# Kernel tuning notes

Measured on AMD Instinct MI355X. Metric: run time of the kernel, lower is better.

The kernel has to match this reference:

```python
import jax, jax.numpy as jnp
import numpy as np

N_NODES = 100000
N_EDGES = 1600000
IN_C, HID_C, OUT_C = 64, 64, 32


def setup_inputs() -> dict:
    key = jax.random.key(0)
    ks = jax.random.split(key, 10)
    return {
        "x": jax.random.normal(ks[0], (N_NODES, IN_C), dtype=jnp.float32),
        "edge_index": jax.random.randint(ks[1], (2, N_EDGES), 0, N_NODES, dtype=jnp.int32),
        "W_l": jax.random.normal(ks[2], (IN_C, HID_C), dtype=jnp.float32) * 0.1,
        "W_r": jax.random.normal(ks[3], (IN_C, HID_C), dtype=jnp.float32) * 0.1,
        "b1": jax.random.normal(ks[4], (HID_C,), dtype=jnp.float32) * 0.1,
        "W_g": jax.random.normal(ks[5], (HID_C, OUT_C), dtype=jnp.float32) * 0.1,
        "att_src": jax.random.normal(ks[6], (OUT_C,), dtype=jnp.float32) * 0.1,
        "att_dst": jax.random.normal(ks[7], (OUT_C,), dtype=jnp.float32) * 0.1,
        "b2": jax.random.normal(ks[8], (OUT_C,), dtype=jnp.float32) * 0.1,
    }


def _gnn(x, edge_index, W_l, W_r, b1, W_g, att_src, att_dst, b2):
    n = x.shape[0]
    src, dst = edge_index[0], edge_index[1]

    # --- SAGEConv: mean neighbor aggregation + root transform ---
    deg = jax.ops.segment_sum(jnp.ones_like(src, dtype=x.dtype), dst, num_segments=n)
    agg = jax.ops.segment_sum(x[src], dst, num_segments=n)  # [N, IN_C]
    agg = agg / jnp.maximum(deg, 1.0)[:, None]
    h = agg @ W_l + b1 + x @ W_r
    h = jax.nn.relu(h)
    # dropout(p=0.5) is identity in eval mode

    # --- GATConv (heads=1), with self-loops (PyG default) ---
    loop = jnp.arange(n, dtype=src.dtype)
    s = jnp.concatenate([src, loop])
    d = jnp.concatenate([dst, loop])
    z = h @ W_g                      # [N, OUT_C]
    a_s = z @ att_src                # [N] per-node source score
    a_d = z @ att_dst                # [N] per-node dest score
    e = jax.nn.leaky_relu(a_s[s] + a_d[d], negative_slope=0.2)  # [E+N]
    # segment softmax over edges grouped by destination node
    m = jax.ops.segment_max(e, d, num_segments=n)
    ex = jnp.exp(e - m[d])
    denom = jax.ops.segment_sum(ex, d, num_segments=n)
    alpha = ex / denom[d]
    out = jax.ops.segment_sum(alpha[:, None] * z[s], d, num_segments=n) + b2

    return jax.nn.log_softmax(out, axis=1)


def reference(x, edge_index, W_l, W_r, b1, W_g, att_src, att_dst, b2):
    return _gnn(x, edge_index, W_l, W_r, b1, W_g, att_src, att_dst, b2)
```

## Files before the change

kernel.cpp:

```cpp
#include <hip/hip_runtime.h>
#include <cstdint>
#include <cstddef>


typedef unsigned short ushort_t;
typedef unsigned int uint_t;
typedef __attribute__((ext_vector_type(8))) short short8;
typedef __attribute__((ext_vector_type(4))) float f32x4;
typedef __attribute__((ext_vector_type(2))) float f32x2;

__device__ inline ushort_t f2bf(float f) {
    uint_t u = __float_as_uint(f);
    uint_t r = (u + 0x7fffu + ((u >> 16) & 1u)) >> 16;
    return (ushort_t)r;
}
__device__ inline float bf_lo(uint_t u) { return __uint_as_float(u << 16); }
__device__ inline float bf_hi(uint_t u) { return __uint_as_float(u & 0xffff0000u); }

#define PART_CHUNK 8192


__global__ __launch_bounds__(256) void k_cnt(const int* __restrict__ ei, int* __restrict__ tot, int E, int NB) {
    __shared__ int h[512];
    int tid = threadIdx.x;
    for (int b = tid; b < NB; b += 256) h[b] = 0;
    __syncthreads();
    int b0 = blockIdx.x * PART_CHUNK;
    int b1 = min(b0 + PART_CHUNK, E);
    for (int j = b0 + tid; j < b1; j += 256) atomicAdd(&h[ei[E + j] >> 8], 1);
    __syncthreads();
    for (int b = tid; b < NB; b += 256) if (h[b]) atomicAdd(&tot[b], h[b]);
}

__global__ __launch_bounds__(256) void k_scan(const int* __restrict__ tot, int* __restrict__ base,
                                              int* __restrict__ gofs, int* __restrict__ rowptr,
                                              int NB, int E, int N) {
    __shared__ int t[256];
    int tid = threadIdx.x;
    int v0 = (2 * tid < NB) ? tot[2 * tid] : 0;
    int v1 = (2 * tid + 1 < NB) ? tot[2 * tid + 1] : 0;
    t[tid] = v0 + v1;
    __syncthreads();
    for (int off = 1; off < 256; off <<= 1) {
        int u = (tid >= off) ? t[tid - off] : 0;
        __syncthreads();
        t[tid] += u;
        __syncthreads();
    }
    int pairExcl = (tid > 0) ? t[tid - 1] : 0;
    if (2 * tid < NB)     { base[2 * tid] = pairExcl;          gofs[2 * tid] = pairExcl; }
    if (2 * tid + 1 < NB) { base[2 * tid + 1] = pairExcl + v0; gofs[2 * tid + 1] = pairExcl + v0; }
    if (tid == 0) { rowptr[N] = E; base[NB] = E; }
}

__global__ __launch_bounds__(256) void k_part(const int* __restrict__ ei, int* __restrict__ gofs,
                                              uint_t* __restrict__ pairs, int E, int NB) {
    __shared__ int h[512];
    __shared__ int ofs[512];
    int tid = threadIdx.x;
    for (int b = tid; b < NB; b += 256) h[b] = 0;
    __syncthreads();
    int b0 = blockIdx.x * PART_CHUNK;
    int b1 = min(b0 + PART_CHUNK, E);
    for (int j = b0 + tid; j < b1; j += 256) atomicAdd(&h[ei[E + j] >> 8], 1);
    __syncthreads();
    for (int b = tid; b < NB; b += 256) ofs[b] = h[b] ? atomicAdd(&gofs[b], h[b]) : 0;
    __syncthreads();
    for (int j = b0 + tid; j < b1; j += 256) {
        int d = ei[E + j], s = ei[j];
        int p = atomicAdd(&ofs[d >> 8], 1);
        pairs[p] = (uint_t)s | ((uint_t)(d & 255) << 24);
    }
}

__global__ __launch_bounds__(256) void k_csr(const uint_t* __restrict__ pairs, const int* __restrict__ base,
                                             int* __restrict__ rowptr, int* __restrict__ csr, int N) {
    __shared__ int h[256];
    __shared__ int s[256];
    int b = blockIdx.x;
    int d0 = b << 8;
    int e0 = base[b], e1 = base[b + 1];
    int tid = threadIdx.x;
    h[tid] = 0;
    __syncthreads();
    for (int j = e0 + tid; j < e1; j += 256) atomicAdd(&h[pairs[j] >> 24], 1);
    __syncthreads();
    int v = h[tid];
    s[tid] = v;
    __syncthreads();
    for (int off = 1; off < 256; off <<= 1) {
        int u = (tid >= off) ? s[tid - off] : 0;
        __syncthreads();
        s[tid] += u;
        __syncthreads();
    }
    int excl = s[tid] - v;
    int d = d0 + tid;
    if (d < N) rowptr[d] = e0 + excl;
    __syncthreads();
    h[tid] = e0 + excl;
    __syncthreads();
    for (int j = e0 + tid; j < e1; j += 256) {
        uint_t p = pairs[j];
        int pos = atomicAdd(&h[p >> 24], 1);
        csr[pos] = (int)(p & 0xffffffu);
    }
}


__global__ __launch_bounds__(256) void k_cvt(const float* __restrict__ x, ushort_t* __restrict__ xh,
                                             unsigned char* __restrict__ xq, int n4) {
    int idx = blockIdx.x * 256 + threadIdx.x;
    if (idx < n4) {
        float4 v = ((const float4*)x)[idx];
        ushort4 o = { f2bf(v.x), f2bf(v.y), f2bf(v.z), f2bf(v.w) };
        ((ushort4*)xh)[idx] = o;
        int r = 0;
        r = __builtin_amdgcn_cvt_pk_fp8_f32(v.x, v.y, r, false);
        r = __builtin_amdgcn_cvt_pk_fp8_f32(v.z, v.w, r, true);
        ((uint_t*)xq)[idx] = (uint_t)r;
    }
}

__global__ __launch_bounds__(256) void k_wcvt(const float* __restrict__ Wl, const float* __restrict__ Wr,
                                              const float* __restrict__ Wg,
                                              ushort_t* __restrict__ Wlrt, ushort_t* __restrict__ Wgt) {
    int t = blockIdx.x * 256 + threadIdx.x;
    if (t < 64 * 128) {
        int n = t >> 7, k = t & 127;
        float v = (k < 64) ? Wl[k * 64 + n] : Wr[(k - 64) * 64 + n];
        Wlrt[n * 128 + k] = f2bf(v);
    }
    if (t < 32 * 64) {
        int n = t >> 6, k = t & 63;
        Wgt[n * 64 + k] = f2bf(Wg[k * 32 + n]);
    }
}


__global__ __launch_bounds__(256) void k_gather(const unsigned char* __restrict__ xq, const int* __restrict__ rowptr,
                                                const int* __restrict__ csr, ushort_t* __restrict__ aggh, int N) {
    int tid = threadIdx.x;
    int l = tid & 15;
    int i = blockIdx.x * 16 + (tid >> 4);
    if (i >= N) return;
    int r0 = rowptr[i], r1 = rowptr[i + 1];
    int deg = r1 - r0;
    const char* xb = (const char*)xq + l * 4;
    float a0 = 0.f, a1 = 0.f, a2 = 0.f, a3 = 0.f;
    int base = r0;

#define GSTEP(t) { \
        int off = __builtin_amdgcn_ds_swizzle(off_l, ((t) << 5) | 0x10); \
        uint_t u = *(const uint_t*)(xb + off); \
        f32x2 p0 = __builtin_amdgcn_cvt_pk_f32_fp8((int)u, false); \
        f32x2 p1 = __builtin_amdgcn_cvt_pk_f32_fp8((int)u, true); \
        a0 += p0.x; a1 += p0.y; a2 += p1.x; a3 += p1.y; }
#define GSTEPP(t) { \
        int off = __builtin_amdgcn_ds_swizzle(off_l, ((t) << 5) | 0x10); \
        if ((t) < cnt) { \
            uint_t u = *(const uint_t*)(xb + off); \
            f32x2 p0 = __builtin_amdgcn_cvt_pk_f32_fp8((int)u, false); \
            f32x2 p1 = __builtin_amdgcn_cvt_pk_f32_fp8((int)u, true); \
            a0 += p0.x; a1 += p0.y; a2 += p1.x; a3 += p1.y; } }

    for (; base + 16 <= r1; base += 16) {
        int off_l = csr[base + l] << 6;
        GSTEP(0)  GSTEP(1)  GSTEP(2)  GSTEP(3)
        GSTEP(4)  GSTEP(5)  GSTEP(6)  GSTEP(7)
        GSTEP(8)  GSTEP(9)  GSTEP(10) GSTEP(11)
        GSTEP(12) GSTEP(13) GSTEP(14) GSTEP(15)
    }
    int cnt = r1 - base;
    if (cnt > 0) {
        int off_l = ((l < cnt) ? csr[base + l] : csr[base]) << 6;
        GSTEPP(0)  GSTEPP(1)  GSTEPP(2)  GSTEPP(3)
        GSTEPP(4)  GSTEPP(5)  GSTEPP(6)  GSTEPP(7)
        GSTEPP(8)  GSTEPP(9)  GSTEPP(10) GSTEPP(11)
        GSTEPP(12) GSTEPP(13) GSTEPP(14) GSTEPP(15)
    }
#undef GSTEP
#undef GSTEPP
    float dn = 1.0f / fmaxf((float)deg, 1.0f);
    ushort4 o = { f2bf(a0 * dn), f2bf(a1 * dn), f2bf(a2 * dn), f2bf(a3 * dn) };
    *(ushort4*)(aggh + (size_t)i * 64 + l * 4) = o;
}


__global__ __launch_bounds__(256) void k_gemm(const ushort_t* __restrict__ aggh, const ushort_t* __restrict__ xh,
                                              const ushort_t* __restrict__ Wlrt, const ushort_t* __restrict__ Wgt,
                                              const float* __restrict__ b1,
                                              const float* __restrict__ att_src, const float* __restrict__ att_dst,
                                              unsigned char* __restrict__ zq, float* __restrict__ a_s,
                                              float* __restrict__ a_d, int N) {
    __shared__ ushort_t Wls[64 * 136];
    __shared__ ushort_t Wgs[32 * 72];
    __shared__ ushort_t hs[64 * 136];
    int tid = threadIdx.x;
    for (int t = tid; t < 64 * 16; t += 256) {
        int n = t >> 4, cq = t & 15;
        *(uint4*)(&Wls[n * 136 + cq * 8]) = *(const uint4*)(&Wlrt[n * 128 + cq * 8]);
    }
    for (int t = tid; t < 32 * 8; t += 256) {
        int n = t >> 3, cq = t & 7;
        *(uint4*)(&Wgs[n * 72 + cq * 8]) = *(const uint4*)(&Wgt[n * 64 + cq * 8]);
    }
    __syncthreads();

    int w = tid >> 6, lane = tid & 63;
    int c = lane & 15, quad = lane >> 4;
    int m0 = blockIdx.x * 64 + w * 16;
    int row = m0 + c;
    bool rowok = row < N;

    f32x4 acc[4] = {};
    #pragma unroll
    for (int kk = 0; kk < 4; ++kk) {
        const ushort_t* Abase = (kk < 2) ? aggh : xh;
        int koff = (kk & 1) * 32 + quad * 8;
        short8 a = {};
        if (rowok) a = *(const short8*)(Abase + (size_t)row * 64 + koff);
        #pragma unroll
        for (int nb = 0; nb < 4; ++nb) {
            short8 b = *(const short8*)(&Wls[(nb * 16 + c) * 136 + kk * 32 + quad * 8]);
            acc[nb] = __builtin_amdgcn_mfma_f32_16x16x32_bf16(a, b, acc[nb], 0, 0, 0);
        }
    }
    ushort_t* hw = &hs[w * 16 * 136];
    #pragma unroll
    for (int nb = 0; nb < 4; ++nb) {
        float bb = b1[nb * 16 + c];
        #pragma unroll
        for (int r = 0; r < 4; ++r) {
            float h = acc[nb][r] + bb;
            hw[(quad * 4 + r) * 136 + nb * 16 + c] = f2bf(fmaxf(h, 0.f));
        }
    }
    f32x4 acc2[2] = {};
    #pragma unroll
    for (int kk = 0; kk < 2; ++kk) {
        short8 a = *(const short8*)(&hw[c * 136 + kk * 32 + quad * 8]);
        #pragma unroll
        for (int nb = 0; nb < 2; ++nb) {
            short8 b = *(const short8*)(&Wgs[(nb * 16 + c) * 72 + kk * 32 + quad * 8]);
            acc2[nb] = __builtin_amdgcn_mfma_f32_16x16x32_bf16(a, b, acc2[nb], 0, 0, 0);
        }
    }
    float as0 = att_src[c], as1 = att_src[16 + c];
    float ad0 = att_dst[c], ad1 = att_dst[16 + c];
    #pragma unroll
    for (int r = 0; r < 4; ++r) {
        int grow = m0 + quad * 4 + r;
        float z0 = acc2[0][r], z1 = acc2[1][r];
        float ps = z0 * as0 + z1 * as1;
        float pd = z0 * ad0 + z1 * ad1;
        #pragma unroll
        for (int off = 8; off; off >>= 1) {
            ps += __shfl_xor(ps, off, 64);
            pd += __shfl_xor(pd, off, 64);
        }
        if (grow < N) {
            int r8 = __builtin_amdgcn_cvt_pk_fp8_f32(z0, z1, 0, false);
            unsigned char* zrow = zq + (size_t)grow * 32;
            zrow[c] = (unsigned char)(r8 & 0xff);
            zrow[16 + c] = (unsigned char)((r8 >> 8) & 0xff);
            if (c == 0) { a_s[grow] = ps; a_d[grow] = pd; }
        }
    }
}


__global__ __launch_bounds__(256) void k_gat(const unsigned char* __restrict__ zq, const float* __restrict__ a_s,
                                             const float* __restrict__ a_d, const int* __restrict__ rowptr,
                                             const int* __restrict__ csr, const float* __restrict__ b2,
                                             float* __restrict__ out, int N) {
    int tid = threadIdx.x;
    int l = tid & 15;
    int i = blockIdx.x * 16 + (tid >> 4);
    if (i >= N) return;
    int r0 = rowptr[i], r1 = rowptr[i + 1];
    float adi = a_d[i], asi = a_s[i];
    const char* zb = (const char*)zq + l * 2;
    float accx = 0.f, accy = 0.f, dsum = 0.f;
    int base = r0;

#define ASTEP(t) { \
        int off = __builtin_amdgcn_ds_swizzle(off_l, ((t) << 5) | 0x10); \
        float w = __int_as_float(__builtin_amdgcn_ds_swizzle(__float_as_int(w_l), ((t) << 5) | 0x10)); \
        uint_t u = *(const ushort_t*)(zb + off); \
        f32x2 p = __builtin_amdgcn_cvt_pk_f32_fp8((int)u, false); \
        accx += w * p.x; \
        accy += w * p.y; }
#define ASTEPP(t) { \
        int off = __builtin_amdgcn_ds_swizzle(off_l, ((t) << 5) | 0x10); \
        float w = __int_as_float(__builtin_amdgcn_ds_swizzle(__float_as_int(w_l), ((t) << 5) | 0x10)); \
        if ((t) < cnt) { \
            uint_t u = *(const ushort_t*)(zb + off); \
            f32x2 p = __builtin_amdgcn_cvt_pk_f32_fp8((int)u, false); \
            accx += w * p.x; \
            accy += w * p.y; } }

    for (; base + 16 <= r1; base += 16) {
        int s_l = csr[base + l];
        float e = a_s[s_l] + adi;
        e = fmaxf(e, 0.2f * e);
        float w_l = __expf(e);
        dsum += w_l;
        int off_l = s_l << 5;
        ASTEP(0)  ASTEP(1)  ASTEP(2)  ASTEP(3)
        ASTEP(4)  ASTEP(5)  ASTEP(6)  ASTEP(7)
        ASTEP(8)  ASTEP(9)  ASTEP(10) ASTEP(11)
        ASTEP(12) ASTEP(13) ASTEP(14) ASTEP(15)
    }
    int cnt = r1 - base;
    if (cnt > 0) {
        int s_l = (l < cnt) ? csr[base + l] : csr[base];
        float w_l = 0.f;
        if (l < cnt) {
            float e = a_s[s_l] + adi;
            e = fmaxf(e, 0.2f * e);
            w_l = __expf(e);
            dsum += w_l;
        }
        int off_l = s_l << 5;
        ASTEPP(0)  ASTEPP(1)  ASTEPP(2)  ASTEPP(3)
        ASTEPP(4)  ASTEPP(5)  ASTEPP(6)  ASTEPP(7)
        ASTEPP(8)  ASTEPP(9)  ASTEPP(10) ASTEPP(11)
        ASTEPP(12) ASTEPP(13) ASTEPP(14) ASTEPP(15)
    }
#undef ASTEP
#undef ASTEPP
    #pragma unroll
    for (int off = 8; off; off >>= 1) dsum += __shfl_xor(dsum, off, 64);
    float es = asi + adi; es = fmaxf(es, 0.2f * es);
    float wse = __expf(es);
    float denom = dsum + wse;
    uint_t us = *(const ushort_t*)((const char*)zq + (size_t)i * 32 + l * 2);
    f32x2 pself = __builtin_amdgcn_cvt_pk_f32_fp8((int)us, false);
    accx += wse * pself.x;
    accy += wse * pself.y;

    float rden = 1.0f / denom;
    float o0 = accx * rden + b2[l * 2];
    float o1 = accy * rden + b2[l * 2 + 1];
    float m2 = fmaxf(o0, o1);
    #pragma unroll
    for (int off = 8; off; off >>= 1) m2 = fmaxf(m2, __shfl_xor(m2, off, 64));
    float ssum = __expf(o0 - m2) + __expf(o1 - m2);
    #pragma unroll
    for (int off = 8; off; off >>= 1) ssum += __shfl_xor(ssum, off, 64);
    float lg = m2 + __logf(ssum);
    float2 r = { o0 - lg, o1 - lg };
    *(float2*)(out + (size_t)i * 32 + l * 2) = r;
}


extern "C" void kernel_launch(void* const* d_in, const int* in_sizes, int n_in,
                              void* d_out, int out_size, void* d_ws, size_t ws_size,
                              hipStream_t stream) {
    const float* x       = (const float*)d_in[0];
    const int*   ei      = (const int*)d_in[1];
    const float* Wl      = (const float*)d_in[2];
    const float* Wr      = (const float*)d_in[3];
    const float* b1      = (const float*)d_in[4];
    const float* Wg      = (const float*)d_in[5];
    const float* att_src = (const float*)d_in[6];
    const float* att_dst = (const float*)d_in[7];
    const float* b2      = (const float*)d_in[8];
    float* out = (float*)d_out;

    int N = in_sizes[0] / 64;
    int E = in_sizes[1] / 2;
    int NB = (N + 255) >> 8;

    char* ws = (char*)d_ws;
    size_t off = 0;
    auto alloc = [&](size_t bytes) { size_t r = off; off += (bytes + 255) & ~(size_t)255; return r; };
    int* tot       = (int*)(ws + alloc((size_t)(NB + 1) * 4));
    int* base      = (int*)(ws + alloc((size_t)(NB + 1) * 4));
    int* gofs      = (int*)(ws + alloc((size_t)(NB + 1) * 4));
    int* rowptr    = (int*)(ws + alloc((size_t)(N + 1) * 4));
    uint_t* pairs  = (uint_t*)(ws + alloc((size_t)E * 4));
    int* csr       = (int*)(ws + alloc((size_t)E * 4));
    ushort_t* xh   = (ushort_t*)(ws + alloc((size_t)N * 64 * 2));
    unsigned char* xq = (unsigned char*)(ws + alloc((size_t)N * 64));
    ushort_t* aggh = (ushort_t*)(ws + alloc((size_t)N * 64 * 2));
    unsigned char* zq = (unsigned char*)(ws + alloc((size_t)N * 32));
    float* a_s     = (float*)(ws + alloc((size_t)N * 4));
    float* a_d     = (float*)(ws + alloc((size_t)N * 4));
    ushort_t* Wlrt = (ushort_t*)(ws + alloc(64 * 128 * 2));
    ushort_t* Wgt  = (ushort_t*)(ws + alloc(32 * 64 * 2));

    (void)hipMemsetAsync(tot, 0, (size_t)NB * 4, stream);

    int nchunk = (E + PART_CHUNK - 1) / PART_CHUNK;
    int n4 = N * 64 / 4;
    k_cnt    <<<nchunk, 256, 0, stream>>>(ei, tot, E, NB);
    k_cvt    <<<(n4 + 255) / 256, 256, 0, stream>>>(x, xh, xq, n4);
    k_wcvt   <<<32, 256, 0, stream>>>(Wl, Wr, Wg, Wlrt, Wgt);
    k_scan   <<<1, 256, 0, stream>>>(tot, base, gofs, rowptr, NB, E, N);
    k_part   <<<nchunk, 256, 0, stream>>>(ei, gofs, pairs, E, NB);
    k_csr    <<<NB, 256, 0, stream>>>(pairs, base, rowptr, csr, N);
    k_gather <<<(N + 15) / 16, 256, 0, stream>>>(xq, rowptr, csr, aggh, N);
    k_gemm   <<<(N + 63) / 64, 256, 0, stream>>>(aggh, xh, Wlrt, Wgt, b1, att_src, att_dst, zq, a_s, a_d, N);
    k_gat    <<<(N + 15) / 16, 256, 0, stream>>>(zq, a_s, a_d, rowptr, csr, b2, out, N);
}
```

Baseline: 229.6 us.

## Fuse preprocessing kernels and merge CSR build with neighbor gather

Merges the count, input conversion and weight conversion kernels into one launch, and fuses the per-bucket CSR construction with the mean-aggregation gather so each block gathers its own 256 nodes right after building their CSR. The gather and GAT loops replace ds_swizzle broadcasts with an LDS scratch buffer and pad invalid lanes with a zeroed dummy row N, which removes the separate tail paths. This cuts launch count and the rowptr reloads, but the fused gather runs only NB (~391) blocks, far fewer than the previous per-16-node grid, so parallelism and latency hiding drop.

```diff
diff --git a/kernel.cpp b/kernel.cpp
--- a/kernel.cpp
+++ b/kernel.cpp
@@ -14,103 +14,21 @@
     uint_t r = (u + 0x7fffu + ((u >> 16) & 1u)) >> 16;
     return (ushort_t)r;
 }
-__device__ inline float bf_lo(uint_t u) { return __uint_as_float(u << 16); }
-__device__ inline float bf_hi(uint_t u) { return __uint_as_float(u & 0xffff0000u); }
 
 #define PART_CHUNK 8192
 
 
-__global__ __launch_bounds__(256) void k_cnt(const int* __restrict__ ei, int* __restrict__ tot, int E, int NB) {
+__global__ __launch_bounds__(256) void k_pre(const float* __restrict__ x, ushort_t* __restrict__ xh,
+                                             unsigned char* __restrict__ xq,
+                                             const int* __restrict__ ei, int* __restrict__ tot,
+                                             const float* __restrict__ Wl, const float* __restrict__ Wr,
+                                             const float* __restrict__ Wg,
+                                             ushort_t* __restrict__ Wlrt, ushort_t* __restrict__ Wgt,
+                                             unsigned char* __restrict__ zq,
+                                             int n4, int E, int NB, int N, int nchunk) {
     __shared__ int h[512];
-    int tid = threadIdx.x;
-    for (int b = tid; b < NB; b += 256) h[b] = 0;
-    __syncthreads();
-    int b0 = blockIdx.x * PART_CHUNK;
-    int b1 = min(b0 + PART_CHUNK, E);
-    for (int j = b0 + tid; j < b1; j += 256) atomicAdd(&h[ei[E + j] >> 8], 1);
-    __syncthreads();
-    for (int b = tid; b < NB; b += 256) if (h[b]) atomicAdd(&tot[b], h[b]);
-}
-
-__global__ __launch_bounds__(256) void k_scan(const int* __restrict__ tot, int* __restrict__ base,
-                                              int* __restrict__ gofs, int* __restrict__ rowptr,
-                                              int NB, int E, int N) {
-    __shared__ int t[256];
-    int tid = threadIdx.x;
-    int v0 = (2 * tid < NB) ? tot[2 * tid] : 0;
-    int v1 = (2 * tid + 1 < NB) ? tot[2 * tid + 1] : 0;
-    t[tid] = v0 + v1;
-    __syncthreads();
-    for (int off = 1; off < 256; off <<= 1) {
-        int u = (tid >= off) ? t[tid - off] : 0;
-        __syncthreads();
-        t[tid] += u;
-        __syncthreads();
-    }
-    int pairExcl = (tid > 0) ? t[tid - 1] : 0;
-    if (2 * tid < NB)     { base[2 * tid] = pairExcl;          gofs[2 * tid] = pairExcl; }
-    if (2 * tid + 1 < NB) { base[2 * tid + 1] = pairExcl + v0; gofs[2 * tid + 1] = pairExcl + v0; }
-    if (tid == 0) { rowptr[N] = E; base[NB] = E; }
-}
-
-__global__ __launch_bounds__(256) void k_part(const int* __restrict__ ei, int* __restrict__ gofs,
-                                              uint_t* __restrict__ pairs, int E, int NB) {
-    __shared__ int h[512];
-    __shared__ int ofs[512];
-    int tid = threadIdx.x;
-    for (int b = tid; b < NB; b += 256) h[b] = 0;
-    __syncthreads();
-    int b0 = blockIdx.x * PART_CHUNK;
-    int b1 = min(b0 + PART_CHUNK, E);
-    for (int j = b0 + tid; j < b1; j += 256) atomicAdd(&h[ei[E + j] >> 8], 1);
-    __syncthreads();
-    for (int b = tid; b < NB; b += 256) ofs[b] = h[b] ? atomicAdd(&gofs[b], h[b]) : 0;
-    __syncthreads();
-    for (int j = b0 + tid; j < b1; j += 256) {
-        int d = ei[E + j], s = ei[j];
-        int p = atomicAdd(&ofs[d >> 8], 1);
-        pairs[p] = (uint_t)s | ((uint_t)(d & 255) << 24);
-    }
-}
-
-__global__ __launch_bounds__(256) void k_csr(const uint_t* __restrict__ pairs, const int* __restrict__ base,
-                                             int* __restrict__ rowptr, int* __restrict__ csr, int N) {
-    __shared__ int h[256];
-    __shared__ int s[256];
-    int b = blockIdx.x;
-    int d0 = b << 8;
-    int e0 = base[b], e1 = base[b + 1];
-    int tid = threadIdx.x;
-    h[tid] = 0;
-    __syncthreads();
-    for (int j = e0 + tid; j < e1; j += 256) atomicAdd(&h[pairs[j] >> 24], 1);
-    __syncthreads();
-    int v = h[tid];
-    s[tid] = v;
-    __syncthreads();
-    for (int off = 1; off < 256; off <<= 1) {
-        int u = (tid >= off) ? s[tid - off] : 0;
-        __syncthreads();
-        s[tid] += u;
-        __syncthreads();
-    }
-    int excl = s[tid] - v;
-    int d = d0 + tid;
-    if (d < N) rowptr[d] = e0 + excl;
-    __syncthreads();
-    h[tid] = e0 + excl;
-    __syncthreads();
-    for (int j = e0 + tid; j < e1; j += 256) {
-        uint_t p = pairs[j];
-        int pos = atomicAdd(&h[p >> 24], 1);
-        csr[pos] = (int)(p & 0xffffffu);
-    }
-}
-
-
-__global__ __launch_bounds__(256) void k_cvt(const float* __restrict__ x, ushort_t* __restrict__ xh,
-                                             unsigned char* __restrict__ xq, int n4) {
-    int idx = blockIdx.x * 256 + threadIdx.x;
+    int bid = blockIdx.x, tid = threadIdx.x;
+    int idx = bid * 256 + tid;
     if (idx < n4) {
         float4 v = ((const float4*)x)[idx];
         ushort4 o = { f2bf(v.x), f2bf(v.y), f2bf(v.z), f2bf(v.w) };
@@ -120,70 +38,139 @@
         r = __builtin_amdgcn_cvt_pk_fp8_f32(v.z, v.w, r, true);
         ((uint_t*)xq)[idx] = (uint_t)r;
     }
-}
-
-__global__ __launch_bounds__(256) void k_wcvt(const float* __restrict__ Wl, const float* __restrict__ Wr,
-                                              const float* __restrict__ Wg,
-                                              ushort_t* __restrict__ Wlrt, ushort_t* __restrict__ Wgt) {
-    int t = blockIdx.x * 256 + threadIdx.x;
-    if (t < 64 * 128) {
+    if (bid < nchunk) {
+        for (int b = tid; b < NB; b += 256) h[b] = 0;
+        __syncthreads();
+        int b0 = bid * PART_CHUNK;
+        int b1 = min(b0 + PART_CHUNK, E);
+        for (int j = b0 + tid; j < b1; j += 256) atomicAdd(&h[ei[E + j] >> 8], 1);
+        __syncthreads();
+        for (int b = tid; b < NB; b += 256) if (h[b]) atomicAdd(&tot[b], h[b]);
+    } else if (bid == nchunk) {
+        if (tid < 16) ((uint_t*)(xq + (size_t)N * 64))[tid] = 0;
+        if (tid < 8)  ((uint_t*)(zq + (size_t)N * 32))[tid] = 0;
+    } else if (bid >= 512 && bid < 544) {
+        int t = (bid - 512) * 256 + tid;
         int n = t >> 7, k = t & 127;
         float v = (k < 64) ? Wl[k * 64 + n] : Wr[(k - 64) * 64 + n];
         Wlrt[n * 128 + k] = f2bf(v);
-    }
-    if (t < 32 * 64) {
-        int n = t >> 6, k = t & 63;
-        Wgt[n * 64 + k] = f2bf(Wg[k * 32 + n]);
-    }
-}
-
-
-__global__ __launch_bounds__(256) void k_gather(const unsigned char* __restrict__ xq, const int* __restrict__ rowptr,
-                                                const int* __restrict__ csr, ushort_t* __restrict__ aggh, int N) {
-    int tid = threadIdx.x;
-    int l = tid & 15;
-    int i = blockIdx.x * 16 + (tid >> 4);
-    if (i >= N) return;
-    int r0 = rowptr[i], r1 = rowptr[i + 1];
-    int deg = r1 - r0;
+        if (t < 32 * 64) {
+            int n2 = t >> 6, k2 = t & 63;
+            Wgt[n2 * 64 + k2] = f2bf(Wg[k2 * 32 + n2]);
+        }
+    }
+}
+
+
+__global__ __launch_bounds__(256) void k_scan(const int* __restrict__ tot, int* __restrict__ base,
+                                              int* __restrict__ gofs, int* __restrict__ rowptr,
+                                              int NB, int E, int N) {
+    __shared__ int t[256];
+    int tid = threadIdx.x;
+    int v0 = (2 * tid < NB) ? tot[2 * tid] : 0;
+    int v1 = (2 * tid + 1 < NB) ? tot[2 * tid + 1] : 0;
+    t[tid] = v0 + v1;
+    __syncthreads();
+    for (int off = 1; off < 256; off <<= 1) {
+        int u = (tid >= off) ? t[tid - off] : 0;
+        __syncthreads();
+        t[tid] += u;
+        __syncthreads();
+    }
+    int pairExcl = (tid > 0) ? t[tid - 1] : 0;
+    if (2 * tid < NB)     { base[2 * tid] = pairExcl;          gofs[2 * tid] = pairExcl; }
+    if (2 * tid + 1 < NB) { base[2 * tid + 1] = pairExcl + v0; gofs[2 * tid + 1] = pairExcl + v0; }
+    if (tid == 0) { rowptr[N] = E; base[NB] = E; }
+}
+
+
+__global__ __launch_bounds__(256) void k_part(const int* __restrict__ ei, int* __restrict__ gofs,
+                                              uint_t* __restrict__ pairs, int E, int NB) {
+    __shared__ int h[512];
+    __shared__ int ofs[512];
+    int tid = threadIdx.x;
+    for (int b = tid; b < NB; b += 256) h[b] = 0;
+    __syncthreads();
+    int b0 = blockIdx.x * PART_CHUNK;
+    int b1 = min(b0 + PART_CHUNK, E);
+    for (int j = b0 + tid; j < b1; j += 256) atomicAdd(&h[ei[E + j] >> 8], 1);
+    __syncthreads();
+    for (int b = tid; b < NB; b += 256) ofs[b] = h[b] ? atomicAdd(&gofs[b], h[b]) : 0;
+    __syncthreads();
+    for (int j = b0 + tid; j < b1; j += 256) {
+        int d = ei[E + j], s = ei[j];
+        int p = atomicAdd(&ofs[d >> 8], 1);
+        pairs[p] = (uint_t)s | ((uint_t)(d & 255) << 24);
+    }
+}
+
+
+__global__ __launch_bounds__(256) void k_csrg(const uint_t* __restrict__ pairs, const int* __restrict__ base,
+                                              int* __restrict__ rowptr, int* __restrict__ csr,
+                                              const unsigned char* __restrict__ xq,
+                                              ushort_t* __restrict__ aggh, int N) {
+    __shared__ int h[256];
+    __shared__ int s[256];
+    __shared__ int scr[256];
+    int b = blockIdx.x;
+    int d0 = b << 8;
+    int e0 = base[b], e1 = base[b + 1];
+    int tid = threadIdx.x;
+    h[tid] = 0;
+    __syncthreads();
+    for (int j = e0 + tid; j < e1; j += 256) atomicAdd(&h[pairs[j] >> 24], 1);
+    __syncthreads();
+    int v = h[tid];
+    s[tid] = v;
+    __syncthreads();
+    for (int off = 1; off < 256; off <<= 1) {
+        int u = (tid >= off) ? s[tid - off] : 0;
+        __syncthreads();
+        s[tid] += u;
+        __syncthreads();
+    }
+    int excl = s[tid] - v;
+    if (d0 + tid < N) rowptr[d0 + tid] = e0 + excl;
+    __syncthreads();
+    h[tid] = e0 + excl;
+    __syncthreads();
+    for (int j = e0 + tid; j < e1; j += 256) {
+        uint_t p = pairs[j];
+        int pos = atomicAdd(&h[p >> 24], 1);
+        csr[pos] = (int)(p & 0xffffffu);
+    }
+    __syncthreads();
+
+    int l = tid & 15, g = tid >> 4;
     const char* xb = (const char*)xq + l * 4;
-    float a0 = 0.f, a1 = 0.f, a2 = 0.f, a3 = 0.f;
-    int base = r0;
-
-#define GSTEP(t) { \
-        int off = __builtin_amdgcn_ds_swizzle(off_l, ((t) << 5) | 0x10); \
-        uint_t u = *(const uint_t*)(xb + off); \
-        f32x2 p0 = __builtin_amdgcn_cvt_pk_f32_fp8((int)u, false); \
-        f32x2 p1 = __builtin_amdgcn_cvt_pk_f32_fp8((int)u, true); \
-        a0 += p0.x; a1 += p0.y; a2 += p1.x; a3 += p1.y; }
-#define GSTEPP(t) { \
-        int off = __builtin_amdgcn_ds_swizzle(off_l, ((t) << 5) | 0x10); \
-        if ((t) < cnt) { \
-            uint_t u = *(const uint_t*)(xb + off); \
-            f32x2 p0 = __builtin_amdgcn_cvt_pk_f32_fp8((int)u, false); \
-            f32x2 p1 = __builtin_amdgcn_cvt_pk_f32_fp8((int)u, true); \
-            a0 += p0.x; a1 += p0.y; a2 += p1.x; a3 += p1.y; } }
-
-    for (; base + 16 <= r1; base += 16) {
-        int off_l = csr[base + l] << 6;
-        GSTEP(0)  GSTEP(1)  GSTEP(2)  GSTEP(3)
-        GSTEP(4)  GSTEP(5)  GSTEP(6)  GSTEP(7)
-        GSTEP(8)  GSTEP(9)  GSTEP(10) GSTEP(11)
-        GSTEP(12) GSTEP(13) GSTEP(14) GSTEP(15)
-    }
-    int cnt = r1 - base;
-    if (cnt > 0) {
-        int off_l = ((l < cnt) ? csr[base + l] : csr[base]) << 6;
-        GSTEPP(0)  GSTEPP(1)  GSTEPP(2)  GSTEPP(3)
-        GSTEPP(4)  GSTEPP(5)  GSTEPP(6)  GSTEPP(7)
-        GSTEPP(8)  GSTEPP(9)  GSTEPP(10) GSTEPP(11)
-        GSTEPP(12) GSTEPP(13) GSTEPP(14) GSTEPP(15)
-    }
-#undef GSTEP
-#undef GSTEPP
-    float dn = 1.0f / fmaxf((float)deg, 1.0f);
-    ushort4 o = { f2bf(a0 * dn), f2bf(a1 * dn), f2bf(a2 * dn), f2bf(a3 * dn) };
-    *(ushort4*)(aggh + (size_t)i * 64 + l * 4) = o;
+    for (int p = 0; p < 16; ++p) {
+        int no = p * 16 + g;
+        int i = d0 + no;
+        if (i >= N) continue;
+        int r0 = e0 + ((no > 0) ? s[no - 1] : 0);
+        int r1 = e0 + s[no];
+        float a0 = 0.f, a1 = 0.f, a2 = 0.f, a3 = 0.f;
+        for (int bb = r0; bb < r1; bb += 16) {
+            int idx = bb + l;
+            int src = (idx < r1) ? csr[idx] : N;
+            scr[tid] = src << 6;
+            #pragma unroll
+            for (int r = 0; r < 4; ++r) {
+                uint4 q = *(const uint4*)&scr[g * 16 + r * 4];
+                #pragma unroll
+                for (int e = 0; e < 4; ++e) {
+                    uint_t off = (e == 0) ? q.x : (e == 1) ? q.y : (e == 2) ? q.z : q.w;
+                    uint_t u = *(const uint_t*)(xb + off);
+                    f32x2 p0 = __builtin_amdgcn_cvt_pk_f32_fp8((int)u, false);
+                    f32x2 p1 = __builtin_amdgcn_cvt_pk_f32_fp8((int)u, true);
+                    a0 += p0.x; a1 += p0.y; a2 += p1.x; a3 += p1.y;
+                }
+            }
+        }
+        float dn = 1.0f / fmaxf((float)(r1 - r0), 1.0f);
+        ushort4 o = { f2bf(a0 * dn), f2bf(a1 * dn), f2bf(a2 * dn), f2bf(a3 * dn) };
+        *(ushort4*)(aggh + (size_t)i * 64 + l * 4) = o;
+    }
 }
 
 
@@ -274,62 +261,45 @@
                                              const float* __restrict__ a_d, const int* __restrict__ rowptr,
                                              const int* __restrict__ csr, const float* __restrict__ b2,
                                              float* __restrict__ out, int N) {
-    int tid = threadIdx.x;
-    int l = tid & 15;
-    int i = blockIdx.x * 16 + (tid >> 4);
+    __shared__ uint2 scr[256];
+    int tid = threadIdx.x;
+    int l = tid & 15, g = tid >> 4;
+    int i = blockIdx.x * 16 + g;
     if (i >= N) return;
     int r0 = rowptr[i], r1 = rowptr[i + 1];
     float adi = a_d[i], asi = a_s[i];
     const char* zb = (const char*)zq + l * 2;
     float accx = 0.f, accy = 0.f, dsum = 0.f;
-    int base = r0;
-
-#define ASTEP(t) { \
-        int off = __builtin_amdgcn_ds_swizzle(off_l, ((t) << 5) | 0x10); \
-        float w = __int_as_float(__builtin_amdgcn_ds_swizzle(__float_as_int(w_l), ((t) << 5) | 0x10)); \
-        uint_t u = *(const ushort_t*)(zb + off); \
-        f32x2 p = __builtin_amdgcn_cvt_pk_f32_fp8((int)u, false); \
-        accx += w * p.x; \
-        accy += w * p.y; }
-#define ASTEPP(t) { \
-        int off = __builtin_amdgcn_ds_swizzle(off_l, ((t) << 5) | 0x10); \
-        float w = __int_as_float(__builtin_amdgcn_ds_swizzle(__float_as_int(w_l), ((t) << 5) | 0x10)); \
-        if ((t) < cnt) { \
-            uint_t u = *(const ushort_t*)(zb + off); \
-            f32x2 p = __builtin_amdgcn_cvt_pk_f32_fp8((int)u, false); \
-            accx += w * p.x; \
-            accy += w * p.y; } }
-
-    for (; base + 16 <= r1; base += 16) {
-        int s_l = csr[base + l];
-        float e = a_s[s_l] + adi;
-        e = fmaxf(e, 0.2f * e);
-        float w_l = __expf(e);
-        dsum += w_l;
-        int off_l = s_l << 5;
-        ASTEP(0)  ASTEP(1)  ASTEP(2)  ASTEP(3)
-        ASTEP(4)  ASTEP(5)  ASTEP(6)  ASTEP(7)
-        ASTEP(8)  ASTEP(9)  ASTEP(10) ASTEP(11)
-        ASTEP(12) ASTEP(13) ASTEP(14) ASTEP(15)
-    }
-    int cnt = r1 - base;
-    if (cnt > 0) {
-        int s_l = (l < cnt) ? csr[base + l] : csr[base];
+
+    for (int bb = r0; bb < r1; bb += 16) {
+        int idx = bb + l;
+        bool valid = idx < r1;
+        int s_l = valid ? csr[idx] : N;
         float w_l = 0.f;
-        if (l < cnt) {
+        if (valid) {
             float e = a_s[s_l] + adi;
             e = fmaxf(e, 0.2f * e);
             w_l = __expf(e);
             dsum += w_l;
         }
-        int off_l = s_l << 5;
-        ASTEPP(0)  ASTEPP(1)  ASTEPP(2)  ASTEPP(3)
-        ASTEPP(4)  ASTEPP(5)  ASTEPP(6)  ASTEPP(7)
-        ASTEPP(8)  ASTEPP(9)  ASTEPP(10) ASTEPP(11)
-        ASTEPP(12) ASTEPP(13) ASTEPP(14) ASTEPP(15)
-    }
-#undef ASTEP
-#undef ASTEPP
+        scr[tid] = make_uint2((uint_t)(s_l << 5), __float_as_uint(w_l));
+        #pragma unroll
+        for (int r = 0; r < 8; ++r) {
+            uint4 q = *(const uint4*)&scr[g * 16 + r * 2];
+            {
+                uint_t u = *(const ushort_t*)(zb + q.x);
+                f32x2 p = __builtin_amdgcn_cvt_pk_f32_fp8((int)u, false);
+                float w = __uint_as_float(q.y);
+                accx += w * p.x; accy += w * p.y;
+            }
+            {
+                uint_t u = *(const ushort_t*)(zb + q.z);
+                f32x2 p = __builtin_amdgcn_cvt_pk_f32_fp8((int)u, false);
+                float w = __uint_as_float(q.w);
+                accx += w * p.x; accy += w * p.y;
+            }
+        }
+    }
     #pragma unroll
     for (int off = 8; off; off >>= 1) dsum += __shfl_xor(dsum, off, 64);
     float es = asi + adi; es = fmaxf(es, 0.2f * es);
@@ -383,9 +353,9 @@
     uint_t* pairs  = (uint_t*)(ws + alloc((size_t)E * 4));
     int* csr       = (int*)(ws + alloc((size_t)E * 4));
     ushort_t* xh   = (ushort_t*)(ws + alloc((size_t)N * 64 * 2));
-    unsigned char* xq = (unsigned char*)(ws + alloc((size_t)N * 64));
+    unsigned char* xq = (unsigned char*)(ws + alloc((size_t)(N + 1) * 64));
     ushort_t* aggh = (ushort_t*)(ws + alloc((size_t)N * 64 * 2));
-    unsigned char* zq = (unsigned char*)(ws + alloc((size_t)N * 32));
+    unsigned char* zq = (unsigned char*)(ws + alloc((size_t)(N + 1) * 32));
     float* a_s     = (float*)(ws + alloc((size_t)N * 4));
     float* a_d     = (float*)(ws + alloc((size_t)N * 4));
     ushort_t* Wlrt = (ushort_t*)(ws + alloc(64 * 128 * 2));
@@ -395,13 +365,12 @@
 
     int nchunk = (E + PART_CHUNK - 1) / PART_CHUNK;
     int n4 = N * 64 / 4;
-    k_cnt    <<<nchunk, 256, 0, stream>>>(ei, tot, E, NB);
-    k_cvt    <<<(n4 + 255) / 256, 256, 0, stream>>>(x, xh, xq, n4);
-    k_wcvt   <<<32, 256, 0, stream>>>(Wl, Wr, Wg, Wlrt, Wgt);
-    k_scan   <<<1, 256, 0, stream>>>(tot, base, gofs, rowptr, NB, E, N);
-    k_part   <<<nchunk, 256, 0, stream>>>(ei, gofs, pairs, E, NB);
-    k_csr    <<<NB, 256, 0, stream>>>(pairs, base, rowptr, csr, N);
-    k_gather <<<(N + 15) / 16, 256, 0, stream>>>(xq, rowptr, csr, aggh, N);
-    k_gemm   <<<(N + 63) / 64, 256, 0, stream>>>(aggh, xh, Wlrt, Wgt, b1, att_src, att_dst, zq, a_s, a_d, N);
-    k_gat    <<<(N + 15) / 16, 256, 0, stream>>>(zq, a_s, a_d, rowptr, csr, b2, out, N);
-}
+    int gpre = (n4 + 255) / 256;
+    if (gpre < 545) gpre = 545;
+    k_pre  <<<gpre, 256, 0, stream>>>(x, xh, xq, ei, tot, Wl, Wr, Wg, Wlrt, Wgt, zq, n4, E, NB, N, nchunk);
+    k_scan <<<1, 256, 0, stream>>>(tot, base, gofs, rowptr, NB, E, N);
+    k_part <<<nchunk, 256, 0, stream>>>(ei, gofs, pairs, E, NB);
+    k_csrg <<<NB, 256, 0, stream>>>(pairs, base, rowptr, csr, xq, aggh, N);
+    k_gemm <<<(N + 63) / 64, 256, 0, stream>>>(aggh, xh, Wlrt, Wgt, b1, att_src, att_dst, zq, a_s, a_d, N);
+    k_gat  <<<(N + 15) / 16, 256, 0, stream>>>(zq, a_s, a_d, rowptr, csr, b2, out, N);
+}
```

Result: faster. 210.7 us (-8.2%).
